# Kernel tuning notes

Measured on AMD Instinct MI355X. Metric: run time of the kernel, lower is better.

The kernel has to match this reference:

```python
import jax, jax.numpy as jnp
import numpy as np

N_NODES = 50000
N_EDGES = 1_600_000
IN_DIM = 512
HIDDEN = 512
OUT_DIM = 128
K = 10
ALPHA = 0.1


def setup_inputs() -> dict:
    key = jax.random.key(0)
    ks = jax.random.split(key, 7)
    x = jax.random.normal(ks[0], (N_NODES, IN_DIM), dtype=jnp.float32)
    edge_index = jax.random.randint(ks[1], (2, N_EDGES), 0, N_NODES, dtype=jnp.int64)
    s_in = 1.0 / np.sqrt(IN_DIM)
    s_h = 1.0 / np.sqrt(HIDDEN)
    lin_in_w = jax.random.uniform(ks[2], (HIDDEN, IN_DIM), jnp.float32, -s_in, s_in)
    lin_in_b = jax.random.uniform(ks[3], (HIDDEN,), jnp.float32, -s_in, s_in)
    lin_out_w = jax.random.uniform(ks[4], (OUT_DIM, HIDDEN), jnp.float32, -s_h, s_h)
    lin_out_b = jax.random.uniform(ks[5], (OUT_DIM,), jnp.float32, -s_h, s_h)
    # GPR init: alpha*(1-alpha)^k, normalized
    w = np.array([ALPHA * (1 - ALPHA) ** k for k in range(K + 1)], dtype=np.float32)
    gpr_weights = jnp.asarray(w / w.sum())
    return {
        "x": x, "edge_index": edge_index,
        "lin_in_w": lin_in_w, "lin_in_b": lin_in_b,
        "lin_out_w": lin_out_w, "lin_out_b": lin_out_b,
        "gpr_weights": gpr_weights,
    }


def reference(x, edge_index, lin_in_w, lin_in_b, lin_out_w, lin_out_b, gpr_weights):
    n = x.shape[0]
    loops = jnp.arange(n, dtype=edge_index.dtype)
    row = jnp.concatenate([edge_index[0], loops])  # [E+n]
    col = jnp.concatenate([edge_index[1], loops])
    # degree over rows (edge_index_sl[0]), clamped to >=1
    deg = jax.ops.segment_sum(jnp.ones_like(row, dtype=x.dtype), row, num_segments=n)
    dis = jnp.clip(deg, 1.0) ** -0.5  # deg^-0.5, [n]

    h = jax.nn.relu(x @ lin_in_w.T + lin_in_b)  # [n, hidden] (dropout = identity in eval)
    w = jax.nn.softmax(gpr_weights)  # [K+1]

    def step(carry, wk):
        h_prop, acc = carry
        hs = h_prop * dis[:, None]
        h_prop = jax.ops.segment_sum(hs[col], row, num_segments=n) * dis[:, None]
        return (h_prop, acc + wk * h_prop), None

    (_, h_final), _ = jax.lax.scan(step, (h, w[0] * h), w[1:])
    return h_final @ lin_out_w.T + lin_out_b
```

## Files before the change

kernel.cpp:

```cpp
#include <hip/hip_runtime.h>


#define SLOTS 96
#define CAP 2688
#define LDP 36

typedef __attribute__((ext_vector_type(8))) short short8;
typedef __attribute__((ext_vector_type(4))) float f32x4;

__device__ inline ushort f2bf(float f) {
    uint x = __float_as_uint(f);
    return (ushort)((x + 0x7fffu + ((x >> 16) & 1u)) >> 16);
}
__device__ inline float bflo(uint u) { return __uint_as_float(u << 16); }
__device__ inline float bfhi(uint u) { return __uint_as_float(u & 0xffff0000u); }

__device__ inline short8 pack8(float4 a, float4 b) {
    short8 o;
    o[0] = (short)f2bf(a.x); o[1] = (short)f2bf(a.y);
    o[2] = (short)f2bf(a.z); o[3] = (short)f2bf(a.w);
    o[4] = (short)f2bf(b.x); o[5] = (short)f2bf(b.y);
    o[6] = (short)f2bf(b.z); o[7] = (short)f2bf(b.w);
    return o;
}

__global__ void init_kernel(int* __restrict__ bcur, int nbc,
                            ushort* __restrict__ yAll, size_t ystride, int zrow,
                            uint* __restrict__ cfill, int cfcnt, uint cfval) {
    const int gid = blockIdx.x * blockDim.x + threadIdx.x;
    const int stride = gridDim.x * blockDim.x;
    for (int i = gid; i < cfcnt; i += stride) cfill[i] = cfval;
    for (int i = gid; i < nbc; i += stride) bcur[i] = 0;
    for (int i = gid; i < 11 * 128; i += stride) {
        int k = i >> 7, d = i & 127;
        yAll[(size_t)k * ystride + (size_t)zrow * 128 + d] = 0;
    }
}

__global__ void bucket_scatter_kernel(const int* __restrict__ row, const int* __restrict__ col,
                                      int* __restrict__ bcur, uint* __restrict__ bbuf, int E) {
    int i = blockIdx.x * blockDim.x + threadIdx.x;
    int stride = gridDim.x * blockDim.x;
    for (; i < E; i += stride) {
        int r = __builtin_nontemporal_load(&row[i]);
        int c = __builtin_nontemporal_load(&col[i]);
        int b = r >> 6;
        int pos = atomicAdd(&bcur[b * 16], 1);
        if (pos < CAP)
            bbuf[(size_t)b * CAP + pos] = ((uint)(r & 63) << 16) | (uint)c;
    }
}

__global__ __launch_bounds__(256) void bucket_expand_kernel(
    const int* __restrict__ bcur, const uint* __restrict__ bbuf,
    ushort* __restrict__ col_s, int* __restrict__ deg,
    float* __restrict__ dis, float* __restrict__ dis2, float* __restrict__ rdis, int n) {
    __shared__ int cur[64];
    const int tid = threadIdx.x;
    const int b = blockIdx.x;
    if (tid < 64) cur[tid] = 0;
    __syncthreads();
    int cb = bcur[b * 16];
    if (cb > CAP) cb = CAP;
    const size_t bb = (size_t)b * CAP;
    for (int i = tid; i < cb; i += 256) {
        uint e = bbuf[bb + i];
        int rl = (int)(e >> 16);
        int pos = atomicAdd(&cur[rl], 1);
        if (pos < SLOTS)
            col_s[((size_t)(b * 64 + rl)) * SLOTS + pos] = (ushort)(e & 0xffffu);
    }
    __syncthreads();
    if (tid < 64) {
        int r = b * 64 + tid;
        if (r < n) {
            int d = cur[tid];
            deg[r] = d;
            float fd = (float)(d + 1);
            float di = rsqrtf(fd);
            dis[r] = di;
            dis2[r] = di * di;
            rdis[r] = sqrtf(fd);
        }
    }
}

__global__ __launch_bounds__(512) void gemm1_kernel(
    const float* __restrict__ X, const float* __restrict__ Wf,
    const float* __restrict__ bias, ushort* __restrict__ outH, int M) {
    __shared__ __align__(16) short As[128 * LDP];
    __shared__ __align__(16) short Bs[256 * LDP];
    const int tid = threadIdx.x;
    const int lane = tid & 63;
    const int wv = tid >> 6;
    const int wm = (wv >> 2) * 64;
    const int wn = (wv & 3) * 64;
    const int bm = blockIdx.y * 128;
    const int bn = blockIdx.x * 256;
    const int lrow = lane & 15;
    const int lk8 = (lane >> 4) * 8;

    f32x4 acc[4][4];
#pragma unroll
    for (int i = 0; i < 4; ++i)
#pragma unroll
        for (int j = 0; j < 4; ++j) acc[i][j] = (f32x4)(0.f);

    const int ra = tid >> 2;
    const int ga = (tid & 3) * 8;
    const int rb = tid >> 1;
    const int gb = (tid & 1) * 16;

    for (int k0 = 0; k0 < 512; k0 += 32) {
        float4 fz = make_float4(0.f, 0.f, 0.f, 0.f);
        float4 f0 = fz, f1 = fz;
        if (bm + ra < M) {
            const float* xp = X + (size_t)(bm + ra) * 512 + k0 + ga;
            f0 = *reinterpret_cast<const float4*>(xp);
            f1 = *reinterpret_cast<const float4*>(xp + 4);
        }
        short8 av = pack8(f0, f1);
        const float* wp = Wf + (size_t)(bn + rb) * 512 + k0 + gb;
        float4 g0 = *reinterpret_cast<const float4*>(wp);
        float4 g1 = *reinterpret_cast<const float4*>(wp + 4);
        float4 g2 = *reinterpret_cast<const float4*>(wp + 8);
        float4 g3 = *reinterpret_cast<const float4*>(wp + 12);
        short8 bv0 = pack8(g0, g1);
        short8 bv1 = pack8(g2, g3);
        __syncthreads();
        *reinterpret_cast<short8*>(As + ra * LDP + ga) = av;
        *reinterpret_cast<short8*>(Bs + rb * LDP + gb) = bv0;
        *reinterpret_cast<short8*>(Bs + rb * LDP + gb + 8) = bv1;
        __syncthreads();
        short8 af[4], bfr[4];
#pragma unroll
        for (int mf = 0; mf < 4; ++mf)
            af[mf] = *reinterpret_cast<const short8*>(As + (wm + mf * 16 + lrow) * LDP + lk8);
#pragma unroll
        for (int nf = 0; nf < 4; ++nf)
            bfr[nf] = *reinterpret_cast<const short8*>(Bs + (wn + nf * 16 + lrow) * LDP + lk8);
#pragma unroll
        for (int mf = 0; mf < 4; ++mf)
#pragma unroll
            for (int nf = 0; nf < 4; ++nf)
                acc[mf][nf] = __builtin_amdgcn_mfma_f32_16x16x32_bf16(af[mf], bfr[nf], acc[mf][nf], 0, 0, 0);
    }

#pragma unroll
    for (int mf = 0; mf < 4; ++mf) {
#pragma unroll
        for (int nf = 0; nf < 4; ++nf) {
            const int col = bn + wn + nf * 16 + lrow;
#pragma unroll
            for (int r = 0; r < 4; ++r) {
                const int row = bm + wm + mf * 16 + (lane >> 4) * 4 + r;
                if (row < M) {
                    float v = fmaxf(acc[mf][nf][r] + bias[col], 0.f);
                    outH[(size_t)row * 512 + col] = f2bf(v);
                }
            }
        }
    }
}

__global__ __launch_bounds__(256) void gemm2_kernel(
    const ushort* __restrict__ H, const float* __restrict__ Wf,
    const float* __restrict__ dis, ushort* __restrict__ outY, int M) {
    __shared__ __align__(16) short As[128 * LDP];
    __shared__ __align__(16) short Bs[128 * LDP];
    const int tid = threadIdx.x;
    const int lane = tid & 63;
    const int wv = tid >> 6;
    const int wm = (wv >> 1) * 64;
    const int wn = (wv & 1) * 64;
    const int bm = blockIdx.x * 128;
    const int lrow = lane & 15;
    const int lk8 = (lane >> 4) * 8;

    f32x4 acc[4][4];
#pragma unroll
    for (int i = 0; i < 4; ++i)
#pragma unroll
        for (int j = 0; j < 4; ++j) acc[i][j] = (f32x4)(0.f);

    const int ra = tid >> 2;
    const int ga = (tid & 3) * 8;
    const int rb = tid >> 1;
    const int gb = (tid & 1) * 16;

    for (int k0 = 0; k0 < 512; k0 += 32) {
        short8 a0 = *reinterpret_cast<const short8*>(H + (size_t)(bm + ra) * 512 + k0 + ga);
        short8 a1 = *reinterpret_cast<const short8*>(H + (size_t)(bm + ra + 64) * 512 + k0 + ga);
        const float* wp = Wf + (size_t)rb * 512 + k0 + gb;
        float4 g0 = *reinterpret_cast<const float4*>(wp);
        float4 g1 = *reinterpret_cast<const float4*>(wp + 4);
        float4 g2 = *reinterpret_cast<const float4*>(wp + 8);
        float4 g3 = *reinterpret_cast<const float4*>(wp + 12);
        short8 bv0 = pack8(g0, g1);
        short8 bv1 = pack8(g2, g3);
        __syncthreads();
        *reinterpret_cast<short8*>(As + ra * LDP + ga) = a0;
        *reinterpret_cast<short8*>(As + (ra + 64) * LDP + ga) = a1;
        *reinterpret_cast<short8*>(Bs + rb * LDP + gb) = bv0;
        *reinterpret_cast<short8*>(Bs + rb * LDP + gb + 8) = bv1;
        __syncthreads();
        short8 af[4], bfr[4];
#pragma unroll
        for (int mf = 0; mf < 4; ++mf)
            af[mf] = *reinterpret_cast<const short8*>(As + (wm + mf * 16 + lrow) * LDP + lk8);
#pragma unroll
        for (int nf = 0; nf < 4; ++nf)
            bfr[nf] = *reinterpret_cast<const short8*>(Bs + (wn + nf * 16 + lrow) * LDP + lk8);
#pragma unroll
        for (int mf = 0; mf < 4; ++mf)
#pragma unroll
            for (int nf = 0; nf < 4; ++nf)
                acc[mf][nf] = __builtin_amdgcn_mfma_f32_16x16x32_bf16(af[mf], bfr[nf], acc[mf][nf], 0, 0, 0);
    }

#pragma unroll
    for (int mf = 0; mf < 4; ++mf) {
#pragma unroll
        for (int nf = 0; nf < 4; ++nf) {
            const int col = wn + nf * 16 + lrow;
#pragma unroll
            for (int r = 0; r < 4; ++r) {
                const int row = bm + wm + mf * 16 + (lane >> 4) * 4 + r;
                if (row < M)
                    outY[(size_t)row * 128 + col] = f2bf(dis[row] * acc[mf][nf][r]);
            }
        }
    }
}

__global__ __launch_bounds__(256) void spmm128_kernel(
    const int* __restrict__ deg, const ushort* __restrict__ col_s,
    const float* __restrict__ dis2,
    const ushort* __restrict__ y_old, ushort* __restrict__ y_new, int n) {
    int wid = (blockIdx.x * 256 + threadIdx.x) >> 6;
    if (wid >= n) return;
    wid = __builtin_amdgcn_readfirstlane(wid);
    const int lane = threadIdx.x & 63;
    int cnt = deg[wid];
    if (cnt > SLOTS) cnt = SLOTS;
    const int cnt16 = (cnt + 15) & ~15;
    const ushort* __restrict__ cp = col_s + (size_t)wid * SLOTS;
    const uint* __restrict__ Y = reinterpret_cast<const uint*>(y_old);
    float s0a = 0.f, s1a = 0.f, s0b = 0.f, s1b = 0.f;
    for (int t = 0; t < cnt16; t += 16) {
        int c[16];
        uint v[16];
#pragma unroll
        for (int j = 0; j < 16; ++j) c[j] = (int)cp[t + j];
#pragma unroll
        for (int j = 0; j < 16; ++j) v[j] = Y[(size_t)c[j] * 64 + lane];
#pragma unroll
        for (int j = 0; j < 16; ++j) {
            if (j & 1) { s0b += bflo(v[j]); s1b += bfhi(v[j]); }
            else       { s0a += bflo(v[j]); s1a += bfhi(v[j]); }
        }
    }
    const uint u = Y[(size_t)wid * 64 + lane];
    const float d2 = dis2[wid];
    const float y0 = d2 * (bflo(u) + (s0a + s0b));
    const float y1 = d2 * (bfhi(u) + (s1a + s1b));
    const uint pv = (uint)f2bf(y0) | ((uint)f2bf(y1) << 16);
    __builtin_nontemporal_store(pv, &reinterpret_cast<uint*>(y_new)[(size_t)wid * 64 + lane]);
}

__global__ __launch_bounds__(256) void finsum_kernel(
    const ushort* __restrict__ yAll, size_t ystride_dw,
    const float* __restrict__ gpr, const float* __restrict__ rdis,
    const float* __restrict__ bout, float* __restrict__ outp, int n) {
    __shared__ float w[11];
    if (threadIdx.x == 0) {
        float m = gpr[0];
        for (int i = 1; i < 11; ++i) m = fmaxf(m, gpr[i]);
        float e[11], s = 0.f;
        for (int i = 0; i < 11; ++i) { e[i] = expf(gpr[i] - m); s += e[i]; }
        float inv = 1.f / s;
        for (int i = 0; i < 11; ++i) w[i] = e[i] * inv;
    }
    __syncthreads();
    const int gid = blockIdx.x * 256 + threadIdx.x;
    if (gid >= n * 64) return;
    const int row = gid >> 6;
    const int lane = gid & 63;
    const uint* __restrict__ Y = reinterpret_cast<const uint*>(yAll);
    float s0 = 0.f, s1 = 0.f;
#pragma unroll
    for (int k = 0; k < 11; ++k) {
        const uint v = Y[k * ystride_dw + (size_t)row * 64 + lane];
        const float wk = w[k];
        s0 = fmaf(wk, bflo(v), s0);
        s1 = fmaf(wk, bfhi(v), s1);
    }
    const float r = rdis[row];
    float2 o;
    o.x = fmaf(s0, r, bout[lane * 2 + 0]);
    o.y = fmaf(s1, r, bout[lane * 2 + 1]);
    *reinterpret_cast<float2*>(outp + (size_t)row * 128 + lane * 2) = o;
}

extern "C" void kernel_launch(void* const* d_in, const int* in_sizes, int n_in,
                              void* d_out, int out_size, void* d_ws, size_t ws_size,
                              hipStream_t stream) {
    const float* x    = (const float*)d_in[0];
    const int*   ei   = (const int*)d_in[1];
    const float* win  = (const float*)d_in[2];
    const float* bin  = (const float*)d_in[3];
    const float* wout = (const float*)d_in[4];
    const float* bout = (const float*)d_in[5];
    const float* gpr  = (const float*)d_in[6];
    float* out = (float*)d_out;

    const int n = in_sizes[0] / 512;
    const int E = in_sizes[1] / 2;
    const int Mpad = ((n + 127) / 128) * 128;
    const int nb = (n + 63) >> 6;

    char* ws = (char*)d_ws;
    size_t off = 0;
    auto take = [&](size_t bytes) -> char* {
        char* p = ws + off;
        off += (bytes + 511) & ~(size_t)511;
        return p;
    };
    int*    deg     = (int*)take((size_t)n * sizeof(int));
    float*  dis     = (float*)take((size_t)n * sizeof(float));
    float*  dis2    = (float*)take((size_t)n * sizeof(float));
    float*  rdis    = (float*)take((size_t)n * sizeof(float));
    int*    bcur    = (int*)take((size_t)nb * 16 * sizeof(int));
    uint*   bbuf    = (uint*)take((size_t)nb * CAP * sizeof(uint));
    ushort* col_s   = (ushort*)take((size_t)n * SLOTS * sizeof(ushort));
    ushort* h_bf    = (ushort*)take((size_t)Mpad * 512 * sizeof(ushort));
    const size_t ystride = (size_t)Mpad * 128;
    ushort* yAll    = (ushort*)take(11 * ystride * sizeof(ushort));

    const int* rowp = ei;
    const int* colp = ei + E;

    init_kernel<<<2048, 256, 0, stream>>>(bcur, nb * 16, yAll, ystride, n,
                                          (uint*)col_s, n * SLOTS / 2,
                                          ((uint)n << 16) | (uint)n);
    bucket_scatter_kernel<<<2048, 256, 0, stream>>>(rowp, colp, bcur, bbuf, E);
    bucket_expand_kernel<<<nb, 256, 0, stream>>>(bcur, bbuf, col_s, deg, dis, dis2, rdis, n);

    dim3 g1(2, Mpad / 128);
    gemm1_kernel<<<g1, 512, 0, stream>>>(x, win, bin, h_bf, n);

    gemm2_kernel<<<Mpad / 128, 256, 0, stream>>>(h_bf, wout, dis, yAll, n);

    const int spmm_blocks = (n + 3) / 4;
    for (int k = 1; k <= 10; ++k) {
        spmm128_kernel<<<spmm_blocks, 256, 0, stream>>>(
            deg, col_s, dis2, yAll + (size_t)(k - 1) * ystride, yAll + (size_t)k * ystride, n);
    }

    finsum_kernel<<<(n * 64 + 255) / 256, 256, 0, stream>>>(
        yAll, ystride / 2, gpr, rdis, bout, out, n);
}
```

Before: 721.8 us.

## Block-local edge partitioning, bf16 pre-conversion, and direct global-to-LDS GEMM loads

Edge bucketing becomes a two-level partition. Each block counts and prefix-sums edges in shared memory into 98 coarse buckets, which cuts global atomics to one per bucket per chunk, and an expand pass then splits each bucket across 4 blocks. A separate kernel pre-converts x and both weight matrices to bf16. Both GEMMs then load tiles with global_load_lds straight into unpadded LDS, dropping the per-tile fp32-to-bf16 packing. The costs are an extra full pass over x, unpadded LDS that may cause bank conflicts, and a fixed NB2/BCAP sizing tied to n=50000.

```diff
diff --git a/kernel.cpp b/kernel.cpp
--- a/kernel.cpp
+++ b/kernel.cpp
@@ -2,8 +2,9 @@
 
 
 #define SLOTS 96
-#define CAP 2688
-#define LDP 36
+#define NB2   98
+#define BCAP  18432
+#define CHUNK 4096
 
 typedef __attribute__((ext_vector_type(8))) short short8;
 typedef __attribute__((ext_vector_type(4))) float f32x4;
@@ -15,64 +16,104 @@
 __device__ inline float bflo(uint u) { return __uint_as_float(u << 16); }
 __device__ inline float bfhi(uint u) { return __uint_as_float(u & 0xffff0000u); }
 
-__device__ inline short8 pack8(float4 a, float4 b) {
-    short8 o;
-    o[0] = (short)f2bf(a.x); o[1] = (short)f2bf(a.y);
-    o[2] = (short)f2bf(a.z); o[3] = (short)f2bf(a.w);
-    o[4] = (short)f2bf(b.x); o[5] = (short)f2bf(b.y);
-    o[6] = (short)f2bf(b.z); o[7] = (short)f2bf(b.w);
-    return o;
-}
-
-__global__ void init_kernel(int* __restrict__ bcur, int nbc,
+__device__ __forceinline__ void glds16(const ushort* g, ushort* l) {
+    __builtin_amdgcn_global_load_lds(
+        (const __attribute__((address_space(1))) void*)g,
+        (__attribute__((address_space(3))) void*)l, 16, 0, 0);
+}
+
+__global__ void init_kernel(int* __restrict__ gcur, int ngc,
                             ushort* __restrict__ yAll, size_t ystride, int zrow,
                             uint* __restrict__ cfill, int cfcnt, uint cfval) {
     const int gid = blockIdx.x * blockDim.x + threadIdx.x;
     const int stride = gridDim.x * blockDim.x;
     for (int i = gid; i < cfcnt; i += stride) cfill[i] = cfval;
-    for (int i = gid; i < nbc; i += stride) bcur[i] = 0;
+    for (int i = gid; i < ngc; i += stride) gcur[i] = 0;
     for (int i = gid; i < 11 * 128; i += stride) {
         int k = i >> 7, d = i & 127;
         yAll[(size_t)k * ystride + (size_t)zrow * 128 + d] = 0;
     }
 }
 
-__global__ void bucket_scatter_kernel(const int* __restrict__ row, const int* __restrict__ col,
-                                      int* __restrict__ bcur, uint* __restrict__ bbuf, int E) {
-    int i = blockIdx.x * blockDim.x + threadIdx.x;
-    int stride = gridDim.x * blockDim.x;
-    for (; i < E; i += stride) {
-        int r = __builtin_nontemporal_load(&row[i]);
-        int c = __builtin_nontemporal_load(&col[i]);
-        int b = r >> 6;
-        int pos = atomicAdd(&bcur[b * 16], 1);
-        if (pos < CAP)
-            bbuf[(size_t)b * CAP + pos] = ((uint)(r & 63) << 16) | (uint)c;
-    }
-}
-
-__global__ __launch_bounds__(256) void bucket_expand_kernel(
-    const int* __restrict__ bcur, const uint* __restrict__ bbuf,
+__global__ __launch_bounds__(512) void partition_kernel(
+    const int* __restrict__ row, const int* __restrict__ col,
+    int* __restrict__ gcur, uint* __restrict__ bbuf, int E) {
+    __shared__ int cnt[128];
+    __shared__ int base[128];
+    __shared__ int gbase[128];
+    __shared__ uint sbuf[CHUNK];
+    const int tid = threadIdx.x;
+    const int e0 = blockIdx.x * CHUNK;
+    if (tid < 128) cnt[tid] = 0;
+    __syncthreads();
+    int myb[8]; int myp[8]; uint mye[8];
+#pragma unroll
+    for (int j = 0; j < 8; ++j) {
+        int i = e0 + tid + j * 512;
+        myb[j] = -1;
+        if (i < E) {
+            int r = row[i];
+            int c = col[i];
+            myb[j] = r >> 9;
+            mye[j] = ((uint)(r & 511) << 16) | (uint)c;
+            myp[j] = atomicAdd(&cnt[myb[j]], 1);
+        }
+    }
+    __syncthreads();
+    if (tid < 128) base[tid] = cnt[tid];
+    __syncthreads();
+    for (int off = 1; off < 128; off <<= 1) {
+        int v = 0;
+        if (tid < 128 && tid >= off) v = base[tid - off];
+        __syncthreads();
+        if (tid < 128) base[tid] += v;
+        __syncthreads();
+    }
+    if (tid < 128) base[tid] -= cnt[tid];
+    __syncthreads();
+    if (tid < NB2 && cnt[tid] > 0) gbase[tid] = atomicAdd(&gcur[tid], cnt[tid]);
+    __syncthreads();
+#pragma unroll
+    for (int j = 0; j < 8; ++j)
+        if (myb[j] >= 0) sbuf[base[myb[j]] + myp[j]] = mye[j];
+    __syncthreads();
+    const int wv = tid >> 6, lane = tid & 63;
+    for (int b = wv; b < NB2; b += 8) {
+        const int len = cnt[b], src = base[b], dst = gbase[b];
+        for (int i = lane; i < len; i += 64) {
+            int d = dst + i;
+            if (d < BCAP) bbuf[(size_t)b * BCAP + d] = sbuf[src + i];
+        }
+    }
+}
+
+__global__ __launch_bounds__(1024) void expand2_kernel(
+    const int* __restrict__ gcur, const uint* __restrict__ bbuf,
     ushort* __restrict__ col_s, int* __restrict__ deg,
-    float* __restrict__ dis, float* __restrict__ dis2, float* __restrict__ rdis, int n) {
-    __shared__ int cur[64];
+    float* __restrict__ dis, float* __restrict__ dis2, float* __restrict__ rdis,
+    int n) {
+    __shared__ int cur[128];
+    const int b = blockIdx.x >> 2;
+    const int q = blockIdx.x & 3;
     const int tid = threadIdx.x;
-    const int b = blockIdx.x;
-    if (tid < 64) cur[tid] = 0;
-    __syncthreads();
-    int cb = bcur[b * 16];
-    if (cb > CAP) cb = CAP;
-    const size_t bb = (size_t)b * CAP;
-    for (int i = tid; i < cb; i += 256) {
+    if (tid < 128) cur[tid] = 0;
+    __syncthreads();
+    int cb = gcur[b];
+    if (cb > BCAP) cb = BCAP;
+    const size_t bb = (size_t)b * BCAP;
+    const int rlo = q * 128, rhi = rlo + 128;
+    for (int i = tid; i < cb; i += 1024) {
         uint e = bbuf[bb + i];
         int rl = (int)(e >> 16);
-        int pos = atomicAdd(&cur[rl], 1);
-        if (pos < SLOTS)
-            col_s[((size_t)(b * 64 + rl)) * SLOTS + pos] = (ushort)(e & 0xffffu);
-    }
-    __syncthreads();
-    if (tid < 64) {
-        int r = b * 64 + tid;
+        if (rl >= rlo && rl < rhi) {
+            int p = atomicAdd(&cur[rl - rlo], 1);
+            if (p < SLOTS)
+                col_s[((size_t)(b * 512 + rl)) * SLOTS + p] = (ushort)(e & 0xffffu);
+        }
+    }
+    __syncthreads();
+    if (tid < 128) {
+        int r = b * 512 + rlo + tid;
         if (r < n) {
             int d = cur[tid];
             deg[r] = d;
@@ -85,20 +126,54 @@
     }
 }
 
+__global__ void cvt_all_kernel(const float* __restrict__ x,
+                               const float* __restrict__ win,
+                               const float* __restrict__ wout,
+                               ushort* __restrict__ x_bf,
+                               ushort* __restrict__ win_bf,
+                               ushort* __restrict__ wout_bf,
+                               int nx_src8, int nx8, int nw18, int nw28) {
+    const int gid = blockIdx.x * blockDim.x + threadIdx.x;
+    const int stride = gridDim.x * blockDim.x;
+    const int tot = nx8 + nw18 + nw28;
+    for (int i = gid; i < tot; i += stride) {
+        const float* src;
+        ushort* dst;
+        int idx;
+        if (i < nx8) {
+            if (i >= nx_src8) {
+                short8 z = (short8)0;
+                *reinterpret_cast<short8*>(x_bf + (size_t)i * 8) = z;
+                continue;
+            }
+            src = x; dst = x_bf; idx = i;
+        } else if (i < nx8 + nw18) {
+            src = win; dst = win_bf; idx = i - nx8;
+        } else {
+            src = wout; dst = wout_bf; idx = i - nx8 - nw18;
+        }
+        const float4* s = reinterpret_cast<const float4*>(src + (size_t)idx * 8);
+        float4 a = s[0], b = s[1];
+        short8 o;
+        o[0] = (short)f2bf(a.x); o[1] = (short)f2bf(a.y);
+        o[2] = (short)f2bf(a.z); o[3] = (short)f2bf(a.w);
+        o[4] = (short)f2bf(b.x); o[5] = (short)f2bf(b.y);
+        o[6] = (short)f2bf(b.z); o[7] = (short)f2bf(b.w);
+        *reinterpret_cast<short8*>(dst + (size_t)idx * 8) = o;
+    }
+}
+
 __global__ __launch_bounds__(512) void gemm1_kernel(
-    const float* __restrict__ X, const float* __restrict__ Wf,
+    const ushort* __restrict__ A, const ushort* __restrict__ B,
     const float* __restrict__ bias, ushort* __restrict__ outH, int M) {
-    __shared__ __align__(16) short As[128 * LDP];
-    __shared__ __align__(16) short Bs[256 * LDP];
+    __shared__ __align__(16) ushort As[128 * 32];
+    __shared__ __align__(16) ushort Bs[256 * 32];
     const int tid = threadIdx.x;
     const int lane = tid & 63;
-    const int wv = tid >> 6;
-    const int wm = (wv >> 2) * 64;
-    const int wn = (wv & 3) * 64;
-    const int bm = blockIdx.y * 128;
-    const int bn = blockIdx.x * 256;
-    const int lrow = lane & 15;
-    const int lk8 = (lane >> 4) * 8;
+    const int w = tid >> 6;
+    const int wm = (w >> 2) * 64, wn = (w & 3) * 64;
+    const int bm = blockIdx.y * 128, bn = blockIdx.x * 256;
+    const int lrow = lane & 15, lk8 = (lane >> 4) * 8;
 
     f32x4 acc[4][4];
 #pragma unroll
@@ -106,44 +181,33 @@
 #pragma unroll
         for (int j = 0; j < 4; ++j) acc[i][j] = (f32x4)(0.f);
 
-    const int ra = tid >> 2;
-    const int ga = (tid & 3) * 8;
-    const int rb = tid >> 1;
-    const int gb = (tid & 1) * 16;
+    const int arow = 16 * w + (lane >> 2);
+    const int acol = (lane & 3) * 8;
+    const ushort* gA = A + (size_t)(bm + arow) * 512 + acol;
+    const ushort* gB0 = B + (size_t)(bn + 32 * w + (lane >> 2)) * 512 + acol;
+    const ushort* gB1 = gB0 + (size_t)16 * 512;
+    ushort* lA = As + w * 512;
+    ushort* lB0 = Bs + w * 1024;
+    ushort* lB1 = Bs + w * 1024 + 512;
 
     for (int k0 = 0; k0 < 512; k0 += 32) {
-        float4 fz = make_float4(0.f, 0.f, 0.f, 0.f);
-        float4 f0 = fz, f1 = fz;
-        if (bm + ra < M) {
-            const float* xp = X + (size_t)(bm + ra) * 512 + k0 + ga;
-            f0 = *reinterpret_cast<const float4*>(xp);
-            f1 = *reinterpret_cast<const float4*>(xp + 4);
-        }
-        short8 av = pack8(f0, f1);
-        const float* wp = Wf + (size_t)(bn + rb) * 512 + k0 + gb;
-        float4 g0 = *reinterpret_cast<const float4*>(wp);
-        float4 g1 = *reinterpret_cast<const float4*>(wp + 4);
-        float4 g2 = *reinterpret_cast<const float4*>(wp + 8);
-        float4 g3 = *reinterpret_cast<const float4*>(wp + 12);
-        short8 bv0 = pack8(g0, g1);
-        short8 bv1 = pack8(g2, g3);
-        __syncthreads();
-        *reinterpret_cast<short8*>(As + ra * LDP + ga) = av;
-        *reinterpret_cast<short8*>(Bs + rb * LDP + gb) = bv0;
-        *reinterpret_cast<short8*>(Bs + rb * LDP + gb + 8) = bv1;
+        glds16(gA + k0, lA);
+        glds16(gB0 + k0, lB0);
+        glds16(gB1 + k0, lB1);
         __syncthreads();
         short8 af[4], bfr[4];
 #pragma unroll
         for (int mf = 0; mf < 4; ++mf)
-            af[mf] = *reinterpret_cast<const short8*>(As + (wm + mf * 16 + lrow) * LDP + lk8);
+            af[mf] = *reinterpret_cast<const short8*>(As + (wm + mf * 16 + lrow) * 32 + lk8);
 #pragma unroll
         for (int nf = 0; nf < 4; ++nf)
-            bfr[nf] = *reinterpret_cast<const short8*>(Bs + (wn + nf * 16 + lrow) * LDP + lk8);
+            bfr[nf] = *reinterpret_cast<const short8*>(Bs + (wn + nf * 16 + lrow) * 32 + lk8);
 #pragma unroll
         for (int mf = 0; mf < 4; ++mf)
 #pragma unroll
             for (int nf = 0; nf < 4; ++nf)
                 acc[mf][nf] = __builtin_amdgcn_mfma_f32_16x16x32_bf16(af[mf], bfr[nf], acc[mf][nf], 0, 0, 0);
+        __syncthreads();
     }
 
 #pragma unroll
@@ -164,18 +228,16 @@
 }
 
 __global__ __launch_bounds__(256) void gemm2_kernel(
-    const ushort* __restrict__ H, const float* __restrict__ Wf,
+    const ushort* __restrict__ A, const ushort* __restrict__ B,
     const float* __restrict__ dis, ushort* __restrict__ outY, int M) {
-    __shared__ __align__(16) short As[128 * LDP];
-    __shared__ __align__(16) short Bs[128 * LDP];
+    __shared__ __align__(16) ushort As[128 * 32];
+    __shared__ __align__(16) ushort Bs[128 * 32];
     const int tid = threadIdx.x;
     const int lane = tid & 63;
-    const int wv = tid >> 6;
-    const int wm = (wv >> 1) * 64;
-    const int wn = (wv & 1) * 64;
+    const int w = tid >> 6;
+    const int wm = (w >> 1) * 64, wn = (w & 1) * 64;
     const int bm = blockIdx.x * 128;
-    const int lrow = lane & 15;
-    const int lk8 = (lane >> 4) * 8;
+    const int lrow = lane & 15, lk8 = (lane >> 4) * 8;
 
     f32x4 acc[4][4];
 #pragma unroll
@@ -183,39 +245,36 @@
 #pragma unroll
         for (int j = 0; j < 4; ++j) acc[i][j] = (f32x4)(0.f);
 
-    const int ra = tid >> 2;
-    const int ga = (tid & 3) * 8;
-    const int rb = tid >> 1;
-    const int gb = (tid & 1) * 16;
+    const int sub = 32 * w + (lane >> 2);
+    const int acol = (lane & 3) * 8;
+    const ushort* gA0 = A + (size_t)(bm + sub) * 512 + acol;
+    const ushort* gA1 = gA0 + (size_t)16 * 512;
+    const ushort* gB0 = B + (size_t)sub * 512 + acol;
+    const ushort* gB1 = gB0 + (size_t)16 * 512;
+    ushort* lA0 = As + w * 1024;
+    ushort* lA1 = As + w * 1024 + 512;
+    ushort* lB0 = Bs + w * 1024;
+    ushort* lB1 = Bs + w * 1024 + 512;
 
     for (int k0 = 0; k0 < 512; k0 += 32) {
-        short8 a0 = *reinterpret_cast<const short8*>(H + (size_t)(bm + ra) * 512 + k0 + ga);
-        short8 a1 = *reinterpret_cast<const short8*>(H + (size_t)(bm + ra + 64) * 512 + k0 + ga);
-        const float* wp = Wf + (size_t)rb * 512 + k0 + gb;
-        float4 g0 = *reinterpret_cast<const float4*>(wp);
-        float4 g1 = *reinterpret_cast<const float4*>(wp + 4);
-        float4 g2 = *reinterpret_cast<const float4*>(wp + 8);
-        float4 g3 = *reinterpret_cast<const float4*>(wp + 12);
-        short8 bv0 = pack8(g0, g1);
-        short8 bv1 = pack8(g2, g3);
-        __syncthreads();
-        *reinterpret_cast<short8*>(As + ra * LDP + ga) = a0;
-        *reinterpret_cast<short8*>(As + (ra + 64) * LDP + ga) = a1;
-        *reinterpret_cast<short8*>(Bs + rb * LDP + gb) = bv0;
-        *reinterpret_cast<short8*>(Bs + rb * LDP + gb + 8) = bv1;
+        glds16(gA0 + k0, lA0);
+        glds16(gA1 + k0, lA1);
+        glds16(gB0 + k0, lB0);
+        glds16(gB1 + k0, lB1);
         __syncthreads();
         short8 af[4], bfr[4];
 #pragma unroll
         for (int mf = 0; mf < 4; ++mf)
-            af[mf] = *reinterpret_cast<const short8*>(As + (wm + mf * 16 + lrow) * LDP + lk8);
+            af[mf] = *reinterpret_cast<const short8*>(As + (wm + mf * 16 + lrow) * 32 + lk8);
 #pragma unroll
         for (int nf = 0; nf < 4; ++nf)
-            bfr[nf] = *reinterpret_cast<const short8*>(Bs + (wn + nf * 16 + lrow) * LDP + lk8);
+            bfr[nf] = *reinterpret_cast<const short8*>(Bs + (wn + nf * 16 + lrow) * 32 + lk8);
 #pragma unroll
         for (int mf = 0; mf < 4; ++mf)
 #pragma unroll
             for (int nf = 0; nf < 4; ++nf)
                 acc[mf][nf] = __builtin_amdgcn_mfma_f32_16x16x32_bf16(af[mf], bfr[nf], acc[mf][nf], 0, 0, 0);
+        __syncthreads();
     }
 
 #pragma unroll
@@ -317,7 +376,7 @@
     const int n = in_sizes[0] / 512;
     const int E = in_sizes[1] / 2;
     const int Mpad = ((n + 127) / 128) * 128;
-    const int nb = (n + 63) >> 6;
+    const int NPAD = NB2 * 512;
 
     char* ws = (char*)d_ws;
     size_t off = 0;
@@ -330,9 +389,12 @@
     float*  dis     = (float*)take((size_t)n * sizeof(float));
     float*  dis2    = (float*)take((size_t)n * sizeof(float));
     float*  rdis    = (float*)take((size_t)n * sizeof(float));
-    int*    bcur    = (int*)take((size_t)nb * 16 * sizeof(int));
-    uint*   bbuf    = (uint*)take((size_t)nb * CAP * sizeof(uint));
-    ushort* col_s   = (ushort*)take((size_t)n * SLOTS * sizeof(ushort));
+    int*    gcur    = (int*)take(128 * sizeof(int));
+    uint*   bbuf    = (uint*)take((size_t)NB2 * BCAP * sizeof(uint));
+    ushort* col_s   = (ushort*)take((size_t)NPAD * SLOTS * sizeof(ushort));
+    ushort* x_bf    = (ushort*)take((size_t)Mpad * 512 * sizeof(ushort));
+    ushort* win_bf  = (ushort*)take((size_t)512 * 512 * sizeof(ushort));
+    ushort* wout_bf = (ushort*)take((size_t)128 * 512 * sizeof(ushort));
     ushort* h_bf    = (ushort*)take((size_t)Mpad * 512 * sizeof(ushort));
     const size_t ystride = (size_t)Mpad * 128;
     ushort* yAll    = (ushort*)take(11 * ystride * sizeof(ushort));
@@ -340,16 +402,19 @@
     const int* rowp = ei;
     const int* colp = ei + E;
 
-    init_kernel<<<2048, 256, 0, stream>>>(bcur, nb * 16, yAll, ystride, n,
-                                          (uint*)col_s, n * SLOTS / 2,
+    init_kernel<<<2048, 256, 0, stream>>>(gcur, 128, yAll, ystride, n,
+                                          (uint*)col_s, NPAD * SLOTS / 2,
                                           ((uint)n << 16) | (uint)n);
-    bucket_scatter_kernel<<<2048, 256, 0, stream>>>(rowp, colp, bcur, bbuf, E);
-    bucket_expand_kernel<<<nb, 256, 0, stream>>>(bcur, bbuf, col_s, deg, dis, dis2, rdis, n);
+    partition_kernel<<<(E + CHUNK - 1) / CHUNK, 512, 0, stream>>>(rowp, colp, gcur, bbuf, E);
+    expand2_kernel<<<NB2 * 4, 1024, 0, stream>>>(gcur, bbuf, col_s, deg, dis, dis2, rdis, n);
+
+    cvt_all_kernel<<<2048, 256, 0, stream>>>(x, win, wout, x_bf, win_bf, wout_bf,
+                                             n * 64, Mpad * 64, 512 * 64, 128 * 64);
 
     dim3 g1(2, Mpad / 128);
-    gemm1_kernel<<<g1, 512, 0, stream>>>(x, win, bin, h_bf, n);
-
-    gemm2_kernel<<<Mpad / 128, 256, 0, stream>>>(h_bf, wout, dis, yAll, n);
+    gemm1_kernel<<<g1, 512, 0, stream>>>(x_bf, win_bf, bin, h_bf, n);
+
+    gemm2_kernel<<<Mpad / 128, 256, 0, stream>>>(h_bf, wout_bf, dis, yAll, n);
 
     const int spmm_blocks = (n + 3) / 4;
     for (int k = 1; k <= 10; ++k) {
```

New measurement: 645.2 us. 1.12x faster.
